# Performance work log

Hardware: AMD Instinct MI355X
Metric: run time of the kernel (lower is better)

## Reference

```python
import jax, jax.numpy as jnp
import numpy as np

ALPHA = 0.1
BETA = 0.3
MARGIN = 2.0


def setup_inputs() -> dict:
    key = jax.random.key(0)
    k1, k2 = jax.random.split(key)
    prediction = jax.random.normal(k1, (8, 2048, 512), dtype=jnp.float32)
    target_seg = jax.random.randint(k2, (8, 2048), 0, 16, dtype=jnp.int64)
    return {"prediction": prediction, "target_seg": target_seg}


def _pairwise_sqdist(x):
    # x: [n, L, d] -> squared Euclidean distances [n, L, L] via a GEMM
    sq = jnp.sum(x * x, axis=-1)  # [n, L]
    inner = jnp.einsum('nld,nmd->nlm', x, x)  # [n, L, L]
    d2 = sq[:, :, None] + sq[:, None, :] - 2.0 * inner
    return jnp.maximum(d2, 0.0)


def _safe_sqrt(d2):
    # sqrt with zero (not NaN) gradient at 0, matching torch.cdist behavior
    pos = d2 > 0
    return jnp.where(pos, jnp.sqrt(jnp.where(pos, d2, 1.0)), 0.0)


def reference(prediction, target_seg):
    # y[i,j,k] = 1 if target_seg[i,j] == target_seg[i,k]
    y = (target_seg[:, :, None] == target_seg[:, None, :]).astype(prediction.dtype)
    d2 = _pairwise_sqdist(prediction)
    dist = _safe_sqrt(d2)
    hinge = jnp.maximum(MARGIN - dist, 0.0)
    loss = ALPHA * y * d2 + BETA * (1.0 - y) * hinge * hinge
    return jnp.mean(loss)
```

## Files before the change

kernel.cpp:

```cpp
#include <hip/hip_runtime.h>
#include <math.h>

#define L      2048
#define DDIM   512
#define NBATCH 8
#define BM     128
#define BN     128
#define BK     64
#define NKT    (DDIM / BK)
#define NTILE  (L / BM)
#define NPAIR  (NTILE * (NTILE + 1) / 2)
#define TOTAL_BLOCKS (NBATCH * NPAIR)

#define ALPHA  0.1f
#define BETA   0.3f
#define MARGIN 2.0f

typedef _Float16 f16x8 __attribute__((ext_vector_type(8)));
typedef __attribute__((ext_vector_type(4))) float f32x4;

#define TILE_SH 8192

#define GLOAD_LDS16(g, l) __builtin_amdgcn_global_load_lds(              \
    (const __attribute__((address_space(1))) unsigned int*)(g),          \
    (__attribute__((address_space(3))) unsigned int*)(l), 16, 0, 0)

__global__ __launch_bounds__(256) void conv_kernel(const float* __restrict__ pred,
                                                   _Float16* __restrict__ h,
                                                   float* __restrict__ sq) {
    int w    = threadIdx.x >> 6;
    int lane = threadIdx.x & 63;
    int row  = blockIdx.x * 4 + w;
    const float* p = pred + (size_t)row * DDIM + lane * 8;
    float4 v0 = *(const float4*)(p);
    float4 v1 = *(const float4*)(p + 4);
    float vals[8] = {v0.x, v0.y, v0.z, v0.w, v1.x, v1.y, v1.z, v1.w};
    f16x8 hv;
    float s = 0.0f;
    #pragma unroll
    for (int i = 0; i < 8; ++i) {
        float x = vals[i];
        s = fmaf(x, x, s);
        hv[i] = (_Float16)x;
    }
    *(f16x8*)(h + (size_t)row * DDIM + lane * 8) = hv;
    #pragma unroll
    for (int off = 32; off > 0; off >>= 1) s += __shfl_down(s, off);
    if (lane == 0) sq[row] = s;
}

__global__ __launch_bounds__(256) void loss_kernel(
        const _Float16* __restrict__ h,
        const int*   __restrict__ seg,
        const float* __restrict__ sq,
        double*      __restrict__ partials) {
    __shared__ _Float16 smem[2 * TILE_SH];
    __shared__ double wred[4];

    int bid = blockIdx.x;
    int n = bid & 7;
    int p = bid >> 3;
    int tj = 0;
    while (true) {
        int rl2 = NTILE - tj;
        if (p < rl2) break;
        p -= rl2;
        ++tj;
    }
    int tk = tj + p;
    int j0 = tj * BM, k0 = tk * BN;

    int t    = threadIdx.x;
    int w    = t >> 6;
    int lane = t & 63;
    int wr   = w >> 1, wc = w & 1;
    int l15  = lane & 15;
    int lq   = lane >> 4;

    const _Float16* baseH = h + (size_t)n * L * DDIM;

    int rl8 = lane >> 3;
    int lc  = (lane & 7) ^ rl8;
    const _Float16* srcA = baseH + (size_t)(j0 + rl8) * DDIM + lc * 8;
    const _Float16* srcB = baseH + (size_t)(k0 + rl8) * DDIM + lc * 8;

    f32x4 acc[4][4];
    #pragma unroll
    for (int m = 0; m < 4; ++m)
        #pragma unroll
        for (int nn = 0; nn < 4; ++nn) acc[m][nn] = (f32x4){0.f, 0.f, 0.f, 0.f};

    #pragma unroll 1
    for (int kt = 0; kt < NKT; ++kt) {
        __syncthreads();
        #pragma unroll
        for (int q = 0; q < 4; ++q) {
            int inst = w * 4 + q;
            GLOAD_LDS16(srcA + (size_t)(inst * 8) * DDIM + kt * BK,
                        smem + inst * 512);
            GLOAD_LDS16(srcB + (size_t)(inst * 8) * DDIM + kt * BK,
                        smem + TILE_SH + inst * 512);
        }
        __syncthreads();

        const _Float16* A = smem;
        const _Float16* B = smem + TILE_SH;

        #pragma unroll
        for (int k2 = 0; k2 < 2; ++k2) {
            int kc = k2 * 4 + lq;
            f16x8 af[4], bf[4];
            #pragma unroll
            for (int m = 0; m < 4; ++m) {
                int R = wr * 64 + m * 16 + l15;
                af[m] = *(const f16x8*)&A[R * 64 + ((kc ^ (R & 7)) << 3)];
            }
            #pragma unroll
            for (int nn = 0; nn < 4; ++nn) {
                int R = wc * 64 + nn * 16 + l15;
                bf[nn] = *(const f16x8*)&B[R * 64 + ((kc ^ (R & 7)) << 3)];
            }
            #pragma unroll
            for (int m = 0; m < 4; ++m)
                #pragma unroll
                for (int nn = 0; nn < 4; ++nn)
                    acc[m][nn] = __builtin_amdgcn_mfma_f32_16x16x32_f16(
                        af[m], bf[nn], acc[m][nn], 0, 0, 0);
        }
    }

    const int*   segb = seg + n * L;
    const float* sqb  = sq + n * L;

    float lsum = 0.0f;
    #pragma unroll
    for (int nn = 0; nn < 4; ++nn) {
        int k = k0 + wc * 64 + nn * 16 + l15;
        float sqk = sqb[k];
        int   sgk = segb[k];
        #pragma unroll
        for (int m = 0; m < 4; ++m)
            #pragma unroll
            for (int reg = 0; reg < 4; ++reg) {
                int j = j0 + wr * 64 + m * 16 + lq * 4 + reg;
                float inner = acc[m][nn][reg];
                float d2 = fmaxf(sqb[j] + sqk - 2.0f * inner, 0.0f);
                float v;
                if (segb[j] == sgk) {
                    v = ALPHA * d2;
                } else {
                    float dist = sqrtf(d2);
                    float hg = fmaxf(MARGIN - dist, 0.0f);
                    v = BETA * hg * hg;
                }
                lsum += v;
            }
    }

    double wgt = (tj == tk) ? 1.0 : 2.0;
    double dsum = (double)lsum * wgt;
    #pragma unroll
    for (int off = 32; off > 0; off >>= 1)
        dsum += __shfl_down(dsum, off);
    if (lane == 0) wred[w] = dsum;
    __syncthreads();
    if (t == 0) partials[bid] = (wred[0] + wred[1]) + (wred[2] + wred[3]);
}

__global__ __launch_bounds__(256) void reduce_kernel(const double* __restrict__ partials,
                                                     float* __restrict__ out,
                                                     int nPart, double invCount) {
    __shared__ double red[256];
    int t = threadIdx.x;
    double s = 0.0;
    for (int i = t; i < nPart; i += 256) s += partials[i];
    red[t] = s;
    __syncthreads();
    #pragma unroll
    for (int k = 128; k > 0; k >>= 1) {
        if (t < k) red[t] += red[t + k];
        __syncthreads();
    }
    if (t == 0) out[0] = (float)(red[0] * invCount);
}

extern "C" void kernel_launch(void* const* d_in, const int* in_sizes, int n_in,
                              void* d_out, int out_size, void* d_ws, size_t ws_size,
                              hipStream_t stream) {
    const float* pred = (const float*)d_in[0];
    const int*   seg  = (const int*)d_in[1];
    float* out = (float*)d_out;

    const size_t HALF = (size_t)NBATCH * L * DDIM;
    _Float16* h        = (_Float16*)d_ws;
    float*    sq       = (float*)(h + HALF);
    double*   partials = (double*)(sq + NBATCH * L);

    conv_kernel<<<NBATCH * L / 4, 256, 0, stream>>>(pred, h, sq);
    loss_kernel<<<TOTAL_BLOCKS, 256, 0, stream>>>(h, seg, sq, partials);
    reduce_kernel<<<1, 256, 0, stream>>>(partials, out, TOTAL_BLOCKS,
                                         1.0 / (double)((size_t)NBATCH * L * L));
}
```

Before: 64.55 us.

## Use 256x256 double-buffered MFMA tiles with 8 waves over the full tile grid

The loss kernel moves from 128x128 tiles with 4 waves and a single LDS buffer to 256x256 tiles with 8 waves. Each k-step prefetches the next tile into a second LDS buffer with direct global-to-LDS loads, and the MFMA work is split into four phases with barriers, sched_barrier and setprio to interleave LDS reads with math. The upper-triangle symmetry trick is dropped: every (j,k) tile is now computed, and there is no ×2 weighting. This gives more reuse per block and hides load latency, but it does about 1.8x more GEMM and epilogue work and needs 128KB of LDS per block, which limits occupancy to one block per CU.

```diff
diff --git a/kernel.cpp b/kernel.cpp
--- a/kernel.cpp
+++ b/kernel.cpp
@@ -4,13 +4,12 @@
 #define L      2048
 #define DDIM   512
 #define NBATCH 8
-#define BM     128
-#define BN     128
+#define BM     256
+#define BN     256
 #define BK     64
 #define NKT    (DDIM / BK)
-#define NTILE  (L / BM)
-#define NPAIR  (NTILE * (NTILE + 1) / 2)
-#define TOTAL_BLOCKS (NBATCH * NPAIR)
+#define NTJ    (L / BM)
+#define TOTAL_BLOCKS (NBATCH * NTJ * NTJ)
 
 #define ALPHA  0.1f
 #define BETA   0.3f
@@ -19,7 +18,9 @@
 typedef _Float16 f16x8 __attribute__((ext_vector_type(8)));
 typedef __attribute__((ext_vector_type(4))) float f32x4;
 
-#define TILE_SH 8192
+#define TILE_SH 16384
+#define BUFSZ   32768
+#define LDS_BYTES (2 * BUFSZ * 2)
 
 #define GLOAD_LDS16(g, l) __builtin_amdgcn_global_load_lds(              \
     (const __attribute__((address_space(1))) unsigned int*)(g),          \
@@ -49,31 +50,25 @@
     if (lane == 0) sq[row] = s;
 }
 
-__global__ __launch_bounds__(256) void loss_kernel(
+__global__ __launch_bounds__(512, 2) void loss_kernel(
         const _Float16* __restrict__ h,
         const int*   __restrict__ seg,
         const float* __restrict__ sq,
         double*      __restrict__ partials) {
-    __shared__ _Float16 smem[2 * TILE_SH];
-    __shared__ double wred[4];
+    extern __shared__ _Float16 smem[];
+    __shared__ double wred[8];
 
     int bid = blockIdx.x;
-    int n = bid & 7;
-    int p = bid >> 3;
-    int tj = 0;
-    while (true) {
-        int rl2 = NTILE - tj;
-        if (p < rl2) break;
-        p -= rl2;
-        ++tj;
-    }
-    int tk = tj + p;
-    int j0 = tj * BM, k0 = tk * BN;
+    int n   = bid & 7;
+    int p   = bid >> 3;
+    int tjj = p >> 3, tkk = p & 7;
+    int j0  = tjj * BM, k0 = tkk * BN;
 
     int t    = threadIdx.x;
-    int w    = t >> 6;
+    int wid  = t >> 6;
     int lane = t & 63;
-    int wr   = w >> 1, wc = w & 1;
+    int wm   = wid >> 2;
+    int wn   = wid & 3;
     int l15  = lane & 15;
     int lq   = lane >> 4;
 
@@ -84,49 +79,123 @@
     const _Float16* srcA = baseH + (size_t)(j0 + rl8) * DDIM + lc * 8;
     const _Float16* srcB = baseH + (size_t)(k0 + rl8) * DDIM + lc * 8;
 
-    f32x4 acc[4][4];
-    #pragma unroll
-    for (int m = 0; m < 4; ++m)
-        #pragma unroll
-        for (int nn = 0; nn < 4; ++nn) acc[m][nn] = (f32x4){0.f, 0.f, 0.f, 0.f};
-
-    #pragma unroll 1
-    for (int kt = 0; kt < NKT; ++kt) {
-        __syncthreads();
-        #pragma unroll
-        for (int q = 0; q < 4; ++q) {
-            int inst = w * 4 + q;
-            GLOAD_LDS16(srcA + (size_t)(inst * 8) * DDIM + kt * BK,
-                        smem + inst * 512);
-            GLOAD_LDS16(srcB + (size_t)(inst * 8) * DDIM + kt * BK,
-                        smem + TILE_SH + inst * 512);
-        }
-        __syncthreads();
-
-        const _Float16* A = smem;
-        const _Float16* B = smem + TILE_SH;
-
-        #pragma unroll
-        for (int k2 = 0; k2 < 2; ++k2) {
-            int kc = k2 * 4 + lq;
-            f16x8 af[4], bf[4];
-            #pragma unroll
-            for (int m = 0; m < 4; ++m) {
-                int R = wr * 64 + m * 16 + l15;
-                af[m] = *(const f16x8*)&A[R * 64 + ((kc ^ (R & 7)) << 3)];
-            }
-            #pragma unroll
-            for (int nn = 0; nn < 4; ++nn) {
-                int R = wc * 64 + nn * 16 + l15;
-                bf[nn] = *(const f16x8*)&B[R * 64 + ((kc ^ (R & 7)) << 3)];
-            }
-            #pragma unroll
-            for (int m = 0; m < 4; ++m)
-                #pragma unroll
-                for (int nn = 0; nn < 4; ++nn)
-                    acc[m][nn] = __builtin_amdgcn_mfma_f32_16x16x32_f16(
-                        af[m], bf[nn], acc[m][nn], 0, 0, 0);
-        }
+    #define STAGE(kt)                                                         \
+    {                                                                         \
+        _Float16* _A = smem + ((kt) & 1) * BUFSZ;                             \
+        _Float16* _B = _A + TILE_SH;                                          \
+        _Pragma("unroll")                                                     \
+        for (int q = 0; q < 4; ++q) {                                         \
+            int inst = wid * 4 + q;                                           \
+            GLOAD_LDS16(srcA + (size_t)(inst * 8) * DDIM + (kt) * BK,         \
+                        _A + inst * 512);                                     \
+            GLOAD_LDS16(srcB + (size_t)(inst * 8) * DDIM + (kt) * BK,         \
+                        _B + inst * 512);                                     \
+        }                                                                     \
+    }
+
+    int x0 = ((0 + lq) ^ (l15 & 7)) << 3;
+    int x1 = ((4 + lq) ^ (l15 & 7)) << 3;
+    int arow[8], brow[4];
+    #pragma unroll
+    for (int mf = 0; mf < 8; ++mf) arow[mf] = (wm * 128 + mf * 16 + l15) * 64;
+    #pragma unroll
+    for (int nf = 0; nf < 4; ++nf) brow[nf] = (wn * 64 + nf * 16 + l15) * 64;
+
+    f32x4 acc[8][4];
+    #pragma unroll
+    for (int mf = 0; mf < 8; ++mf)
+        #pragma unroll
+        for (int nf = 0; nf < 4; ++nf) acc[mf][nf] = (f32x4){0.f, 0.f, 0.f, 0.f};
+
+    STAGE(0);
+
+    #pragma unroll 2
+    for (int j = 0; j < NKT; ++j) {
+        const _Float16* A = smem + (j & 1) * BUFSZ;
+        const _Float16* B = A + TILE_SH;
+
+        asm volatile("s_waitcnt vmcnt(0)" ::: "memory");
+        __builtin_amdgcn_s_barrier();
+        f16x8 a[4][2], b01[2][2];
+        #pragma unroll
+        for (int mf = 0; mf < 4; ++mf) {
+            a[mf][0] = *(const f16x8*)&A[arow[mf] + x0];
+            a[mf][1] = *(const f16x8*)&A[arow[mf] + x1];
+        }
+        #pragma unroll
+        for (int nf = 0; nf < 2; ++nf) {
+            b01[nf][0] = *(const f16x8*)&B[brow[nf] + x0];
+            b01[nf][1] = *(const f16x8*)&B[brow[nf] + x1];
+        }
+        if (j + 1 < NKT) STAGE(j + 1);
+        asm volatile("s_waitcnt lgkmcnt(0)" ::: "memory");
+        __builtin_amdgcn_sched_barrier(0);
+        __builtin_amdgcn_s_setprio(1);
+        #pragma unroll
+        for (int mf = 0; mf < 4; ++mf)
+            #pragma unroll
+            for (int nf = 0; nf < 2; ++nf) {
+                acc[mf][nf] = __builtin_amdgcn_mfma_f32_16x16x32_f16(
+                    a[mf][0], b01[nf][0], acc[mf][nf], 0, 0, 0);
+                acc[mf][nf] = __builtin_amdgcn_mfma_f32_16x16x32_f16(
+                    a[mf][1], b01[nf][1], acc[mf][nf], 0, 0, 0);
+            }
+        __builtin_amdgcn_s_setprio(0);
+
+        __builtin_amdgcn_s_barrier();
+        f16x8 b23[2][2];
+        #pragma unroll
+        for (int nf = 0; nf < 2; ++nf) {
+            b23[nf][0] = *(const f16x8*)&B[brow[nf + 2] + x0];
+            b23[nf][1] = *(const f16x8*)&B[brow[nf + 2] + x1];
+        }
+        asm volatile("s_waitcnt lgkmcnt(0)" ::: "memory");
+        __builtin_amdgcn_sched_barrier(0);
+        __builtin_amdgcn_s_setprio(1);
+        #pragma unroll
+        for (int mf = 0; mf < 4; ++mf)
+            #pragma unroll
+            for (int nf = 0; nf < 2; ++nf) {
+                acc[mf][nf + 2] = __builtin_amdgcn_mfma_f32_16x16x32_f16(
+                    a[mf][0], b23[nf][0], acc[mf][nf + 2], 0, 0, 0);
+                acc[mf][nf + 2] = __builtin_amdgcn_mfma_f32_16x16x32_f16(
+                    a[mf][1], b23[nf][1], acc[mf][nf + 2], 0, 0, 0);
+            }
+        __builtin_amdgcn_s_setprio(0);
+
+        __builtin_amdgcn_s_barrier();
+        f16x8 a2[4][2];
+        #pragma unroll
+        for (int mf = 0; mf < 4; ++mf) {
+            a2[mf][0] = *(const f16x8*)&A[arow[mf + 4] + x0];
+            a2[mf][1] = *(const f16x8*)&A[arow[mf + 4] + x1];
+        }
+        asm volatile("s_waitcnt lgkmcnt(0)" ::: "memory");
+        __builtin_amdgcn_sched_barrier(0);
+        __builtin_amdgcn_s_setprio(1);
+        #pragma unroll
+        for (int mf = 0; mf < 4; ++mf)
+            #pragma unroll
+            for (int nf = 0; nf < 2; ++nf) {
+                acc[mf + 4][nf + 2] = __builtin_amdgcn_mfma_f32_16x16x32_f16(
+                    a2[mf][0], b23[nf][0], acc[mf + 4][nf + 2], 0, 0, 0);
+                acc[mf + 4][nf + 2] = __builtin_amdgcn_mfma_f32_16x16x32_f16(
+                    a2[mf][1], b23[nf][1], acc[mf + 4][nf + 2], 0, 0, 0);
+            }
+        __builtin_amdgcn_s_setprio(0);
+
+        __builtin_amdgcn_s_barrier();
+        __builtin_amdgcn_s_setprio(1);
+        #pragma unroll
+        for (int mf = 0; mf < 4; ++mf)
+            #pragma unroll
+            for (int nf = 0; nf < 2; ++nf) {
+                acc[mf + 4][nf] = __builtin_amdgcn_mfma_f32_16x16x32_f16(
+                    a2[mf][0], b01[nf][0], acc[mf + 4][nf], 0, 0, 0);
+                acc[mf + 4][nf] = __builtin_amdgcn_mfma_f32_16x16x32_f16(
+                    a2[mf][1], b01[nf][1], acc[mf + 4][nf], 0, 0, 0);
+            }
+        __builtin_amdgcn_s_setprio(0);
     }
 
     const int*   segb = seg + n * L;
@@ -134,19 +203,19 @@
 
     float lsum = 0.0f;
     #pragma unroll
-    for (int nn = 0; nn < 4; ++nn) {
-        int k = k0 + wc * 64 + nn * 16 + l15;
+    for (int nf = 0; nf < 4; ++nf) {
+        int k = k0 + wn * 64 + nf * 16 + l15;
         float sqk = sqb[k];
         int   sgk = segb[k];
         #pragma unroll
-        for (int m = 0; m < 4; ++m)
+        for (int mf = 0; mf < 8; ++mf)
             #pragma unroll
             for (int reg = 0; reg < 4; ++reg) {
-                int j = j0 + wr * 64 + m * 16 + lq * 4 + reg;
-                float inner = acc[m][nn][reg];
-                float d2 = fmaxf(sqb[j] + sqk - 2.0f * inner, 0.0f);
+                int jj = j0 + wm * 128 + mf * 16 + lq * 4 + reg;
+                float inner = acc[mf][nf][reg];
+                float d2 = fmaxf(sqb[jj] + sqk - 2.0f * inner, 0.0f);
                 float v;
-                if (segb[j] == sgk) {
+                if (segb[jj] == sgk) {
                     v = ALPHA * d2;
                 } else {
                     float dist = sqrtf(d2);
@@ -157,14 +226,17 @@
             }
     }
 
-    double wgt = (tj == tk) ? 1.0 : 2.0;
-    double dsum = (double)lsum * wgt;
+    double dsum = (double)lsum;
     #pragma unroll
     for (int off = 32; off > 0; off >>= 1)
         dsum += __shfl_down(dsum, off);
-    if (lane == 0) wred[w] = dsum;
+    if (lane == 0) wred[wid] = dsum;
     __syncthreads();
-    if (t == 0) partials[bid] = (wred[0] + wred[1]) + (wred[2] + wred[3]);
+    if (t == 0) {
+        double s = ((wred[0] + wred[1]) + (wred[2] + wred[3]))
+                 + ((wred[4] + wred[5]) + (wred[6] + wred[7]));
+        partials[bid] = s;
+    }
 }
 
 __global__ __launch_bounds__(256) void reduce_kernel(const double* __restrict__ partials,
@@ -196,8 +268,12 @@
     float*    sq       = (float*)(h + HALF);
     double*   partials = (double*)(sq + NBATCH * L);
 
+    (void)hipFuncSetAttribute((const void*)loss_kernel,
+                              hipFuncAttributeMaxDynamicSharedMemorySize,
+                              LDS_BYTES);
+
     conv_kernel<<<NBATCH * L / 4, 256, 0, stream>>>(pred, h, sq);
-    loss_kernel<<<TOTAL_BLOCKS, 256, 0, stream>>>(h, seg, sq, partials);
+    loss_kernel<<<TOTAL_BLOCKS, 512, LDS_BYTES, stream>>>(h, seg, sq, partials);
     reduce_kernel<<<1, 256, 0, stream>>>(partials, out, TOTAL_BLOCKS,
                                          1.0 / (double)((size_t)NBATCH * L * L));
 }
```

After: 76.22 us. 1.18x slower.
